# Kernel optimization log

Hardware: AMD Instinct MI355X
Metric: run time of the kernel (lower is better)

The kernel has to match this reference:

```python
import jax, jax.numpy as jnp
import numpy as np
import math

TOPK = 13
ALPHA = 1.0
BETA = 6.0
EPS = 1e-9
NUM_CLASSES = 80
BG = NUM_CLASSES
IMG = 640.0


def _make_centers():
    # YOLO-style anchor-free grid at strides 8/16/32 for a 640x640 image -> L=8400
    pts = []
    for s, g in [(8, 80), (16, 40), (32, 20)]:
        xs = (np.arange(g) + 0.5) * s
        xv, yv = np.meshgrid(xs, xs)
        pts.append(np.stack([xv.ravel(), yv.ravel()], axis=-1))
    return jnp.asarray(np.concatenate(pts, 0), jnp.float32)


def _rand_boxes(kc, kw, shape, wmin, wmax):
    c = jax.random.uniform(kc, shape + (2,), minval=0.0, maxval=IMG)
    wh = jax.random.uniform(kw, shape + (2,), minval=wmin, maxval=wmax)
    return jnp.concatenate([c - wh / 2, c + wh / 2], axis=-1)


def setup_inputs() -> dict:
    key = jax.random.key(0)
    ks = jax.random.split(key, 8)
    B, L, C, n = 32, 8400, NUM_CLASSES, 64
    centers = _make_centers()                       # (L,2)
    pred_scores = jax.random.uniform(ks[0], (B, L, C))
    # predicted boxes centered near the grid cells
    noise = jax.random.normal(ks[1], (B, L, 2)) * 8.0
    pwh = jax.random.uniform(ks[2], (B, L, 2), minval=4.0, maxval=128.0)
    pc = centers[None] + noise
    pred_bboxes = jnp.concatenate([pc - pwh / 2, pc + pwh / 2], axis=-1)
    gt_bboxes = _rand_boxes(ks[3], ks[4], (B, n), 8.0, 256.0)
    gt_labels = jax.random.randint(ks[5], (B, n, 1), 0, NUM_CLASSES).astype(jnp.int32)
    counts = jax.random.randint(ks[6], (B,), 1, n + 1)
    pad_gt_mask = (jnp.arange(n)[None, :] < counts[:, None]).astype(jnp.float32)[..., None]
    return {"pred_scores": pred_scores, "pred_bboxes": pred_bboxes,
            "cell_centers_scaled": centers, "gt_labels": gt_labels,
            "gt_bboxes": gt_bboxes, "pad_gt_mask": pad_gt_mask}


def _ciou(b1, b2, eps=1e-7):
    # pairwise complete IoU: b1 (n,4) gt, b2 (L,4) pred -> (n,L). Matches torchvision.complete_box_iou.
    a1 = (b1[:, 2] - b1[:, 0]) * (b1[:, 3] - b1[:, 1])
    a2 = (b2[:, 2] - b2[:, 0]) * (b2[:, 3] - b2[:, 1])
    lt = jnp.maximum(b1[:, None, :2], b2[None, :, :2])
    rb = jnp.minimum(b1[:, None, 2:], b2[None, :, 2:])
    wh = jnp.clip(rb - lt, 0)
    inter = wh[..., 0] * wh[..., 1]
    union = a1[:, None] + a2[None, :] - inter
    iou = inter / union
    lti = jnp.minimum(b1[:, None, :2], b2[None, :, :2])
    rbi = jnp.maximum(b1[:, None, 2:], b2[None, :, 2:])
    whi = jnp.clip(rbi - lti, 0)
    diag2 = whi[..., 0] ** 2 + whi[..., 1] ** 2 + eps
    cx1 = (b1[:, 0] + b1[:, 2]) / 2; cy1 = (b1[:, 1] + b1[:, 3]) / 2
    cx2 = (b2[:, 0] + b2[:, 2]) / 2; cy2 = (b2[:, 1] + b2[:, 3]) / 2
    dist2 = (cx1[:, None] - cx2[None, :]) ** 2 + (cy1[:, None] - cy2[None, :]) ** 2
    diou = iou - dist2 / diag2
    w1 = b1[:, 2] - b1[:, 0]; h1 = b1[:, 3] - b1[:, 1]
    w2 = b2[:, 2] - b2[:, 0]; h2 = b2[:, 3] - b2[:, 1]
    v = (4.0 / math.pi ** 2) * (jnp.arctan(w1 / h1)[:, None] - jnp.arctan(w2 / h2)[None, :]) ** 2
    alpha = jax.lax.stop_gradient(v / (1 - iou + v + eps))
    return diou - alpha * v


def reference(pred_scores, pred_bboxes, cell_centers_scaled, gt_labels, gt_bboxes, pad_gt_mask):
    B, L, C = pred_scores.shape
    n = gt_bboxes.shape[1]
    # --- points-inside-gt check: (B,n,L) ---
    x = cell_centers_scaled[None, None, :, 0]
    y = cell_centers_scaled[None, None, :, 1]
    bb = gt_bboxes[:, :, None, :]
    ltrb_min = jnp.minimum(jnp.minimum(x - bb[..., 0], y - bb[..., 1]),
                           jnp.minimum(bb[..., 2] - x, bb[..., 3] - y))
    is_in_gts = (ltrb_min > EPS).astype(gt_bboxes.dtype)        # (B,n,L)
    # --- CIoU between each gt and each pred box ---
    ious = jax.vmap(_ciou)(gt_bboxes, pred_bboxes)              # (B,n,L)
    ious = jnp.clip(jnp.nan_to_num(ious, nan=0.0), 0)
    ious = ious * pad_gt_mask * is_in_gts
    # --- gather class score of each gt's label for every cell ---
    ps_t = jnp.swapaxes(pred_scores, 1, 2)                      # (B,C,L)
    gl = gt_labels.astype(jnp.int32)                            # (B,n,1)
    bbox_cls_scores = jnp.take_along_axis(ps_t, jnp.broadcast_to(gl, (B, n, L)), axis=1)
    alignment_metrics = bbox_cls_scores ** ALPHA * ious ** BETA # (B,n,L)
    # --- topk per gt, one-hot-sum style membership ---
    _, topk_idxs = jax.lax.top_k(alignment_metrics, TOPK)       # (B,n,TOPK)
    topk_mask = jnp.broadcast_to(pad_gt_mask > 0, topk_idxs.shape)
    topk_idxs = jnp.where(topk_mask, topk_idxs, 0)
    bi = jnp.arange(B)[:, None, None]
    ni = jnp.arange(n)[None, :, None]
    cnt = jnp.zeros((B, n, L), jnp.int32).at[bi, ni, topk_idxs].add(1)
    is_in_topk = jnp.where(cnt > 1, 0, cnt).astype(alignment_metrics.dtype)
    mask_positive = is_in_topk * is_in_gts * pad_gt_mask        # (B,n,L)
    mask_positive_sum = mask_positive.sum(axis=1)               # (B,L)
    # --- resolve cells assigned to multiple gts by max IoU (unconditional == torch's data-dependent branch) ---
    is_max_iou = (ious == ious.max(axis=1, keepdims=True)).astype(ious.dtype)
    mask_positive = jnp.where(mask_positive_sum[:, None, :] > 1, is_max_iou, mask_positive)
    mask_positive_sum = mask_positive.sum(axis=1)
    assigned_gt_index = jnp.argmax(mask_positive, axis=1)       # (B,L)
    assigned_labels = jnp.take_along_axis(gl[..., 0], assigned_gt_index, axis=1)
    assigned_labels = jnp.where(mask_positive_sum > 0, assigned_labels, BG)
    assigned_bboxes = jnp.take_along_axis(gt_bboxes, assigned_gt_index[..., None], axis=1)  # (B,L,4)
    assigned_scores = jax.nn.one_hot(assigned_labels, NUM_CLASSES + 1, dtype=pred_scores.dtype)[:, :, :NUM_CLASSES]
    # --- rescale scores by normalized alignment metric ---
    am = alignment_metrics * mask_positive
    max_metrics = am.max(axis=-1, keepdims=True)
    max_ious = (ious * mask_positive).max(axis=-1, keepdims=True)
    am = am / (max_metrics + EPS) * max_ious
    norm = am.max(axis=1)[..., None]                            # (B,L,1)
    assigned_scores = assigned_scores * norm
    foreground_mask = mask_positive_sum > 0
    return assigned_labels, assigned_bboxes, assigned_scores, foreground_mask
```

## Files before the change

### kernel.cpp

```cpp
#include <hip/hip_runtime.h>

#define BATCH 32
#define LANCH 8400
#define NCLS  80
#define NGT   64
#define TOPK  13
#define NCHUNK 33
#define CAP   2048

struct GtLds {
  float4 box[NGT];
  float  ga[NGT], gcx[NGT], gcy[NGT], atg[NGT], padf[NGT];
  int    lab[NGT];
};

__device__ __forceinline__ void load_gt(GtLds& s, int b,
    const float* gt_bboxes, const int* gt_labels, const float* pad_mask, int t)
{
  if (t < NGT) {
    float4 g = reinterpret_cast<const float4*>(gt_bboxes)[b * NGT + t];
    s.box[t] = g;
    float gw = g.z - g.x, gh = g.w - g.y;
    s.ga[t]  = gw * gh;
    s.gcx[t] = (g.x + g.z) * 0.5f;
    s.gcy[t] = (g.y + g.w) * 0.5f;
    s.atg[t] = atanf(gw / gh);
    s.padf[t] = pad_mask[b * NGT + t];
    s.lab[t]  = gt_labels[b * NGT + t];
  }
}

__device__ __forceinline__ float ciou_core(
    float4 pb, float pa, float pcx, float pcy, float atp,
    float4 gb, float ga, float gcx, float gcy, float atg)
{
  float iw = fmaxf(fminf(gb.z, pb.z) - fmaxf(gb.x, pb.x), 0.f);
  float ih = fmaxf(fminf(gb.w, pb.w) - fmaxf(gb.y, pb.y), 0.f);
  float inter = iw * ih;
  float uni   = ga + pa - inter;
  float iou   = inter / uni;
  float wi = fmaxf(fmaxf(gb.z, pb.z) - fminf(gb.x, pb.x), 0.f);
  float hi = fmaxf(fmaxf(gb.w, pb.w) - fminf(gb.y, pb.y), 0.f);
  float diag2 = wi * wi + hi * hi + 1e-7f;
  float dx = gcx - pcx, dy = gcy - pcy;
  float diou = iou - (dx * dx + dy * dy) / diag2;
  float dat = atg - atp;
  float v = 0.40528473456935109f * dat * dat;
  float alpha = v / (1.f - iou + v + 1e-7f);
  return fmaxf(diou - alpha * v, 0.f);
}

__device__ __forceinline__ float masked_ciou(
    float4 pb, float pa, float pcx, float pcy, float atp, float2 cc,
    float4 gb, float ga, float gcx, float gcy, float atg, float padf)
{
  float ltrb = fminf(fminf(cc.x - gb.x, cc.y - gb.y),
                     fminf(gb.z - cc.x, gb.w - cc.y));
  if (!(ltrb > 1e-9f) || padf == 0.f) return 0.f;
  return ciou_core(pb, pa, pcx, pcy, atp, gb, ga, gcx, gcy, atg);
}

__device__ __forceinline__ unsigned long long umax64(unsigned long long a,
                                                     unsigned long long b)
{ return a > b ? a : b; }

__global__ __launch_bounds__(64) void k_rowtopk(
    const float* __restrict__ pred_scores,
    const float* __restrict__ pred_bboxes,
    const float* __restrict__ centers,
    const int*   __restrict__ gt_labels,
    const float* __restrict__ gt_bboxes,
    const float* __restrict__ pad_mask,
    unsigned long long* __restrict__ mask64)
{
  const int bg = blockIdx.x;
  if (pad_mask[bg] == 0.f) return;
  const int b = bg >> 6, g = bg & 63, lane = threadIdx.x;

  __shared__ unsigned long long s_keys[CAP];
  __shared__ int s_winl[TOPK];

  const float4 gt = reinterpret_cast<const float4*>(gt_bboxes)[bg];
  const int   lab = gt_labels[bg];
  const float gw = gt.z - gt.x, gh = gt.w - gt.y;
  const float ga = gw * gh;
  const float gcx = (gt.x + gt.z) * 0.5f, gcy = (gt.y + gt.w) * 0.5f;
  const float atg = atanf(gw / gh);

  const int gdim[3] = {80, 40, 20};
  const int base[3] = {0, 6400, 8000};
  const float inv[3] = {0.125f, 0.0625f, 0.03125f};
  int i0[3], j0[3], w_[3], cum[4]; cum[0] = 0;
  for (int k = 0; k < 3; ++k) {
    int a0 = (int)floorf(gt.x * inv[k] - 0.5f) - 1; a0 = a0 < 0 ? 0 : a0;
    int a1 = (int)ceilf (gt.z * inv[k] - 0.5f) + 1; a1 = a1 > gdim[k] - 1 ? gdim[k] - 1 : a1;
    int b0 = (int)floorf(gt.y * inv[k] - 0.5f) - 1; b0 = b0 < 0 ? 0 : b0;
    int b1 = (int)ceilf (gt.w * inv[k] - 0.5f) + 1; b1 = b1 > gdim[k] - 1 ? gdim[k] - 1 : b1;
    i0[k] = a0; j0[k] = b0;
    int ww = a1 >= a0 ? a1 - a0 + 1 : 0;
    int hh = b1 >= b0 ? b1 - b0 + 1 : 0;
    w_[k] = ww;
    cum[k + 1] = cum[k] + ww * hh;
  }
  const int total = cum[3];
  const float2* cc2 = reinterpret_cast<const float2*>(centers);
  const float4* pb4 = reinterpret_cast<const float4*>(pred_bboxes) + (size_t)b * LANCH;
  const float*  sc  = pred_scores + (size_t)b * LANCH * NCLS + lab;

  int cnt = 0;
  const unsigned long long lmask = (1ull << lane) - 1ull;
  const int iters = (total + 63) >> 6;
  for (int it = 0; it < iters; ++it) {
    const int c = it * 64 + lane;
    bool valid = false;
    unsigned long long key = 0;
    if (c < total) {
      int k = (c >= cum[1]) + (c >= cum[2]);
      int r = c - cum[k];
      int di = r % w_[k], dj = r / w_[k];
      int l = base[k] + (j0[k] + dj) * gdim[k] + (i0[k] + di);
      float2 cc = cc2[l];
      float ltrb = fminf(fminf(cc.x - gt.x, cc.y - gt.y),
                         fminf(gt.z - cc.x, gt.w - cc.y));
      if (ltrb > 1e-9f) {
        float4 pb = pb4[l];
        float pw = pb.z - pb.x, ph = pb.w - pb.y, pa = pw * ph;
        float pcx = (pb.x + pb.z) * 0.5f, pcy = (pb.y + pb.w) * 0.5f;
        float atp = atanf(pw / ph);
        float io = ciou_core(pb, pa, pcx, pcy, atp, gt, ga, gcx, gcy, atg);
        float t2 = io * io;
        float met = sc[(size_t)l * NCLS] * (t2 * t2 * t2);
        if (met > 0.f) {
          valid = true;
          key = ((unsigned long long)__float_as_uint(met) << 32)
              | (unsigned int)(0x7FFFFFFF - l);
        }
      }
    }
    unsigned long long bal = __ballot(valid);
    if (valid) s_keys[cnt + __popcll(bal & lmask)] = key;
    cnt += __popcll(bal);
  }
  const int nnz  = cnt;
  const int npos = nnz < TOPK ? nnz : TOPK;

  unsigned long long mybest = 0;
  for (int i = lane; i < nnz; i += 64) mybest = umax64(mybest, s_keys[i]);

  for (int it = 0; it < npos; ++it) {
    unsigned long long k = mybest;
    #pragma unroll
    for (int off = 32; off > 0; off >>= 1) {
      unsigned long long o = __shfl_xor(k, off);
      if (o > k) k = o;
    }
    if (lane == 0) s_winl[it] = 0x7FFFFFFF - (int)(unsigned int)(k & 0xFFFFFFFFu);
    if (mybest == k) {
      mybest = 0;
      for (int i = lane; i < nnz; i += 64) {
        unsigned long long v = s_keys[i];
        if (v == k) { s_keys[i] = 0; v = 0; }
        mybest = umax64(mybest, v);
      }
    }
  }
  if (lane == 0 && npos < TOPK) {
    int found = npos;
    for (int l = 0; found < TOPK && l < LANCH; ++l) {
      bool taken = false;
      for (int k = 0; k < npos; ++k) if (s_winl[k] == l) taken = true;
      if (!taken) s_winl[found++] = l;
    }
  }
  __syncthreads();
  if (lane < TOPK) {
    int l = s_winl[lane];
    float2 cc = cc2[l];
    float ltrb = fminf(fminf(cc.x - gt.x, cc.y - gt.y),
                       fminf(gt.z - cc.x, gt.w - cc.y));
    if (ltrb > 1e-9f)
      atomicOr(&mask64[(size_t)b * LANCH + l], 1ull << g);
  }
}

__global__ __launch_bounds__(256) void k_resolve(
    const float* __restrict__ pred_scores,
    const float* __restrict__ pred_bboxes,
    const float* __restrict__ centers,
    const int*   __restrict__ gt_labels,
    const float* __restrict__ gt_bboxes,
    const float* __restrict__ pad_mask,
    unsigned long long* __restrict__ mask64,
    float*       __restrict__ ws_mm,
    float*       __restrict__ ws_mi)
{
  __shared__ GtLds s;
  const int b = blockIdx.y, t = threadIdx.x;
  load_gt(s, b, gt_bboxes, gt_labels, pad_mask, t);
  __syncthreads();
  const int l = blockIdx.x * 256 + t;
  if (l >= LANCH) return;
  const int idx = b * LANCH + l;

  unsigned long long mb = mask64[idx];
  if (mb == 0ull) return;
  const int sum1 = __popcll(mb);

  const float4 pb = reinterpret_cast<const float4*>(pred_bboxes)[(size_t)b * LANCH + l];
  const float2 cc = reinterpret_cast<const float2*>(centers)[l];
  const float pw = pb.z - pb.x, ph = pb.w - pb.y;
  const float pa = pw * ph;
  const float pcx = (pb.x + pb.z) * 0.5f, pcy = (pb.y + pb.w) * 0.5f;
  const float atp = atanf(pw / ph);
  const float* srow = pred_scores + ((size_t)b * LANCH + l) * NCLS;

  unsigned long long fb = mb;
  if (sum1 > 1) {
    float mx = 0.f;
    unsigned long long eq = 0;
    for (int g = 0; g < NGT; ++g) {
      if (s.padf[g] == 0.f) break;
      float io = masked_ciou(pb, pa, pcx, pcy, atp, cc, s.box[g],
                             s.ga[g], s.gcx[g], s.gcy[g], s.atg[g], s.padf[g]);
      if (io > mx)       { mx = io; eq = 1ull << g; }
      else if (io == mx) { eq |= 1ull << g; }
    }
    fb = eq;
    mask64[idx] = eq;
  }

  unsigned long long bits = fb;
  while (bits) {
    int g = __ffsll((unsigned long long)bits) - 1;
    bits &= bits - 1;
    float io = masked_ciou(pb, pa, pcx, pcy, atp, cc, s.box[g],
                           s.ga[g], s.gcx[g], s.gcy[g], s.atg[g], s.padf[g]);
    float t2 = io * io;
    float met = srow[s.lab[g]] * (t2 * t2 * t2);
    atomicMax(reinterpret_cast<int*>(ws_mm + b * NGT + g), __float_as_int(met));
    atomicMax(reinterpret_cast<int*>(ws_mi + b * NGT + g), __float_as_int(io));
  }
}

__global__ __launch_bounds__(256) void k_write(
    const float* __restrict__ pred_scores,
    const float* __restrict__ pred_bboxes,
    const float* __restrict__ centers,
    const int*   __restrict__ gt_labels,
    const float* __restrict__ gt_bboxes,
    const float* __restrict__ pad_mask,
    const unsigned long long* __restrict__ mask64,
    const float* __restrict__ ws_mm,
    const float* __restrict__ ws_mi,
    float*       __restrict__ out_labels,
    float*       __restrict__ out_bboxes,
    float*       __restrict__ out_fg,
    float*       __restrict__ out_scores)
{
  __shared__ GtLds s;
  __shared__ float smm[NGT], smi[NGT];
  __shared__ float s_norm[256];
  __shared__ int   s_lab[256];
  const int b = blockIdx.y, t = threadIdx.x;
  load_gt(s, b, gt_bboxes, gt_labels, pad_mask, t);
  if (t < NGT) { smm[t] = ws_mm[b * NGT + t]; smi[t] = ws_mi[b * NGT + t]; }
  __syncthreads();
  const int l0 = blockIdx.x * 256;
  const int l  = l0 + t;
  const bool act = (l < LANCH);

  float norm = 0.f;
  int   lab  = NCLS;
  if (act) {
    const int idx = b * LANCH + l;
    unsigned long long bits = mask64[idx];
    if (bits != 0ull) {
      const float4 pb = reinterpret_cast<const float4*>(pred_bboxes)[(size_t)b * LANCH + l];
      const float2 cc = reinterpret_cast<const float2*>(centers)[l];
      const float pw = pb.z - pb.x, ph = pb.w - pb.y;
      const float pa = pw * ph;
      const float pcx = (pb.x + pb.z) * 0.5f, pcy = (pb.y + pb.w) * 0.5f;
      const float atp = atanf(pw / ph);
      const float* srow = pred_scores + ((size_t)b * LANCH + l) * NCLS;
      const int first = __ffsll((unsigned long long)bits) - 1;
      lab = s.lab[first];
      unsigned long long bb = bits;
      while (bb) {
        int g = __ffsll((unsigned long long)bb) - 1;
        bb &= bb - 1;
        float io = masked_ciou(pb, pa, pcx, pcy, atp, cc, s.box[g],
                               s.ga[g], s.gcx[g], s.gcy[g], s.atg[g], s.padf[g]);
        float t2 = io * io;
        float met = srow[s.lab[g]] * (t2 * t2 * t2);
        norm = fmaxf(norm, met / (smm[g] + 1e-9f) * smi[g]);
      }
      out_labels[idx] = (float)lab;
      reinterpret_cast<float4*>(out_bboxes)[idx] = s.box[first];
      out_fg[idx] = 1.f;
    } else {
      out_labels[idx] = (float)NCLS;
      reinterpret_cast<float4*>(out_bboxes)[idx] = s.box[0];
      out_fg[idx] = 0.f;
    }
  }
  s_norm[t] = norm;
  s_lab[t]  = lab;
  __syncthreads();

  const int QC = NCLS / 4;
  float4* tile = reinterpret_cast<float4*>(out_scores + ((size_t)b * LANCH + l0) * NCLS);
  const int amax = (LANCH - l0) < 256 ? (LANCH - l0) : 256;
  #pragma unroll
  for (int k = 0; k < QC; ++k) {
    int p = k * 256 + t;
    int a = p / QC, c4 = p - a * QC;
    if (a < amax) {
      float4 wv = make_float4(0.f, 0.f, 0.f, 0.f);
      int la = s_lab[a], base = c4 * 4;
      if (la >= base && la < base + 4) (&wv.x)[la - base] = s_norm[a];
      tile[p] = wv;
    }
  }
}

extern "C" void kernel_launch(void* const* d_in, const int* in_sizes, int n_in,
                              void* d_out, int out_size, void* d_ws, size_t ws_size,
                              hipStream_t stream) {
  const float* pred_scores = (const float*)d_in[0];
  const float* pred_bboxes = (const float*)d_in[1];
  const float* centers     = (const float*)d_in[2];
  const int*   gt_labels   = (const int*)  d_in[3];
  const float* gt_bboxes   = (const float*)d_in[4];
  const float* pad_mask    = (const float*)d_in[5];

  char* ws = (char*)d_ws;
  unsigned long long* mask64 = (unsigned long long*)ws;
  float* ws_mm = (float*)(ws + (size_t)BATCH * LANCH * 8);
  float* ws_mi = ws_mm + BATCH * NGT;
  const size_t zero_bytes = (size_t)BATCH * LANCH * 8 + 2 * BATCH * NGT * sizeof(float);

  float* out        = (float*)d_out;
  float* out_labels = out;
  float* out_bboxes = out + (size_t)BATCH * LANCH;
  float* out_scores = out + (size_t)BATCH * LANCH * 5;
  float* out_fg     = out + (size_t)BATCH * LANCH * 5 + (size_t)BATCH * LANCH * NCLS;

  hipMemsetAsync(ws, 0, zero_bytes, stream);

  k_rowtopk<<<BATCH * NGT, 64, 0, stream>>>(pred_scores, pred_bboxes, centers,
      gt_labels, gt_bboxes, pad_mask, mask64);

  dim3 grid(NCHUNK, BATCH);
  k_resolve<<<grid, 256, 0, stream>>>(pred_scores, pred_bboxes, centers,
      gt_labels, gt_bboxes, pad_mask, mask64, ws_mm, ws_mi);

  k_write<<<grid, 256, 0, stream>>>(pred_scores, pred_bboxes, centers,
      gt_labels, gt_bboxes, pad_mask, mask64, ws_mm, ws_mi,
      out_labels, out_bboxes, out_fg, out_scores);
}
```

Measured before the change: 230.3 us.

## Resolve per-batch masks in LDS and pack results for a lean write kernel

```diff
diff --git a/kernel.cpp b/kernel.cpp
--- a/kernel.cpp
+++ b/kernel.cpp
@@ -71,11 +71,11 @@
     const int*   __restrict__ gt_labels,
     const float* __restrict__ gt_bboxes,
     const float* __restrict__ pad_mask,
-    unsigned long long* __restrict__ mask64)
+    int*         __restrict__ ws_top)
 {
   const int bg = blockIdx.x;
   if (pad_mask[bg] == 0.f) return;
-  const int b = bg >> 6, g = bg & 63, lane = threadIdx.x;
+  const int b = bg >> 6, lane = threadIdx.x;
 
   __shared__ unsigned long long s_keys[CAP];
   __shared__ int s_winl[TOPK];
@@ -178,8 +178,7 @@
     float2 cc = cc2[l];
     float ltrb = fminf(fminf(cc.x - gt.x, cc.y - gt.y),
                        fminf(gt.z - cc.x, gt.w - cc.y));
-    if (ltrb > 1e-9f)
-      atomicOr(&mask64[(size_t)b * LANCH + l], 1ull << g);
+    ws_top[bg * 16 + lane] = l | ((ltrb > 1e-9f) ? 0x40000000 : 0);
   }
 }
 
@@ -190,118 +189,129 @@
     const int*   __restrict__ gt_labels,
     const float* __restrict__ gt_bboxes,
     const float* __restrict__ pad_mask,
-    unsigned long long* __restrict__ mask64,
-    float*       __restrict__ ws_mm,
-    float*       __restrict__ ws_mi)
-{
+    const int*   __restrict__ ws_top,
+    unsigned long long* __restrict__ ws_pack)
+{
+  __shared__ unsigned long long s_mask[LANCH];
   __shared__ GtLds s;
-  const int b = blockIdx.y, t = threadIdx.x;
+  __shared__ int s_mm[NGT], s_mi[NGT];
+  const int b = blockIdx.x, t = threadIdx.x;
   load_gt(s, b, gt_bboxes, gt_labels, pad_mask, t);
-  __syncthreads();
-  const int l = blockIdx.x * 256 + t;
-  if (l >= LANCH) return;
-  const int idx = b * LANCH + l;
-
-  unsigned long long mb = mask64[idx];
-  if (mb == 0ull) return;
-  const int sum1 = __popcll(mb);
-
-  const float4 pb = reinterpret_cast<const float4*>(pred_bboxes)[(size_t)b * LANCH + l];
-  const float2 cc = reinterpret_cast<const float2*>(centers)[l];
-  const float pw = pb.z - pb.x, ph = pb.w - pb.y;
-  const float pa = pw * ph;
-  const float pcx = (pb.x + pb.z) * 0.5f, pcy = (pb.y + pb.w) * 0.5f;
-  const float atp = atanf(pw / ph);
-  const float* srow = pred_scores + ((size_t)b * LANCH + l) * NCLS;
-
-  unsigned long long fb = mb;
-  if (sum1 > 1) {
-    float mx = 0.f;
-    unsigned long long eq = 0;
-    for (int g = 0; g < NGT; ++g) {
-      if (s.padf[g] == 0.f) break;
+  if (t < NGT) { s_mm[t] = 0; s_mi[t] = 0; }
+  for (int i = t; i < LANCH; i += 256) s_mask[i] = 0ull;
+  __syncthreads();
+
+  for (int p = t; p < NGT * TOPK; p += 256) {
+    int g = p / TOPK, k = p - g * TOPK;
+    if (s.padf[g] == 0.f) continue;
+    int e = ws_top[(b * NGT + g) * 16 + k];
+    if (e & 0x40000000) atomicOr(&s_mask[e & 0x3FFF], 1ull << g);
+  }
+  __syncthreads();
+
+  const float2* cc2 = reinterpret_cast<const float2*>(centers);
+  const float4* pb4 = reinterpret_cast<const float4*>(pred_bboxes) + (size_t)b * LANCH;
+
+  for (int l = t; l < LANCH; l += 256) {
+    unsigned long long mb = s_mask[l];
+    if (!mb) continue;
+    const float4 pb = pb4[l];
+    const float2 cc = cc2[l];
+    const float pw = pb.z - pb.x, ph = pb.w - pb.y;
+    const float pa = pw * ph;
+    const float pcx = (pb.x + pb.z) * 0.5f, pcy = (pb.y + pb.w) * 0.5f;
+    const float atp = atanf(pw / ph);
+    const float* srow = pred_scores + ((size_t)b * LANCH + l) * NCLS;
+
+    unsigned long long fb = mb;
+    if (__popcll(mb) > 1) {
+      float mx = 0.f;
+      unsigned long long eq = 0;
+      for (int g = 0; g < NGT; ++g) {
+        if (s.padf[g] == 0.f) break;
+        float io = masked_ciou(pb, pa, pcx, pcy, atp, cc, s.box[g],
+                               s.ga[g], s.gcx[g], s.gcy[g], s.atg[g], s.padf[g]);
+        if (io > mx)       { mx = io; eq = 1ull << g; }
+        else if (io == mx) { eq |= 1ull << g; }
+      }
+      fb = eq;
+      s_mask[l] = eq;
+    }
+    unsigned long long bits = fb;
+    while (bits) {
+      int g = __ffsll((unsigned long long)bits) - 1;
+      bits &= bits - 1;
       float io = masked_ciou(pb, pa, pcx, pcy, atp, cc, s.box[g],
                              s.ga[g], s.gcx[g], s.gcy[g], s.atg[g], s.padf[g]);
-      if (io > mx)       { mx = io; eq = 1ull << g; }
-      else if (io == mx) { eq |= 1ull << g; }
-    }
-    fb = eq;
-    mask64[idx] = eq;
-  }
-
-  unsigned long long bits = fb;
-  while (bits) {
-    int g = __ffsll((unsigned long long)bits) - 1;
-    bits &= bits - 1;
-    float io = masked_ciou(pb, pa, pcx, pcy, atp, cc, s.box[g],
-                           s.ga[g], s.gcx[g], s.gcy[g], s.atg[g], s.padf[g]);
-    float t2 = io * io;
-    float met = srow[s.lab[g]] * (t2 * t2 * t2);
-    atomicMax(reinterpret_cast<int*>(ws_mm + b * NGT + g), __float_as_int(met));
-    atomicMax(reinterpret_cast<int*>(ws_mi + b * NGT + g), __float_as_int(io));
-  }
-}
-
-__global__ __launch_bounds__(256) void k_write(
-    const float* __restrict__ pred_scores,
-    const float* __restrict__ pred_bboxes,
-    const float* __restrict__ centers,
-    const int*   __restrict__ gt_labels,
-    const float* __restrict__ gt_bboxes,
-    const float* __restrict__ pad_mask,
-    const unsigned long long* __restrict__ mask64,
-    const float* __restrict__ ws_mm,
-    const float* __restrict__ ws_mi,
-    float*       __restrict__ out_labels,
-    float*       __restrict__ out_bboxes,
-    float*       __restrict__ out_fg,
-    float*       __restrict__ out_scores)
-{
-  __shared__ GtLds s;
-  __shared__ float smm[NGT], smi[NGT];
-  __shared__ float s_norm[256];
-  __shared__ int   s_lab[256];
-  const int b = blockIdx.y, t = threadIdx.x;
-  load_gt(s, b, gt_bboxes, gt_labels, pad_mask, t);
-  if (t < NGT) { smm[t] = ws_mm[b * NGT + t]; smi[t] = ws_mi[b * NGT + t]; }
-  __syncthreads();
-  const int l0 = blockIdx.x * 256;
-  const int l  = l0 + t;
-  const bool act = (l < LANCH);
-
-  float norm = 0.f;
-  int   lab  = NCLS;
-  if (act) {
-    const int idx = b * LANCH + l;
-    unsigned long long bits = mask64[idx];
-    if (bits != 0ull) {
-      const float4 pb = reinterpret_cast<const float4*>(pred_bboxes)[(size_t)b * LANCH + l];
-      const float2 cc = reinterpret_cast<const float2*>(centers)[l];
+      float t2 = io * io;
+      float met = srow[s.lab[g]] * (t2 * t2 * t2);
+      atomicMax(&s_mm[g], __float_as_int(met));
+      atomicMax(&s_mi[g], __float_as_int(io));
+    }
+  }
+  __syncthreads();
+
+  for (int l = t; l < LANCH; l += 256) {
+    unsigned long long mb = s_mask[l];
+    unsigned long long pk = (unsigned long long)NCLS << 16;
+    if (mb) {
+      const float4 pb = pb4[l];
+      const float2 cc = cc2[l];
       const float pw = pb.z - pb.x, ph = pb.w - pb.y;
       const float pa = pw * ph;
       const float pcx = (pb.x + pb.z) * 0.5f, pcy = (pb.y + pb.w) * 0.5f;
       const float atp = atanf(pw / ph);
       const float* srow = pred_scores + ((size_t)b * LANCH + l) * NCLS;
-      const int first = __ffsll((unsigned long long)bits) - 1;
-      lab = s.lab[first];
-      unsigned long long bb = bits;
-      while (bb) {
-        int g = __ffsll((unsigned long long)bb) - 1;
-        bb &= bb - 1;
+      const int first = __ffsll((unsigned long long)mb) - 1;
+      float norm = 0.f;
+      unsigned long long bits = mb;
+      while (bits) {
+        int g = __ffsll((unsigned long long)bits) - 1;
+        bits &= bits - 1;
         float io = masked_ciou(pb, pa, pcx, pcy, atp, cc, s.box[g],
                                s.ga[g], s.gcx[g], s.gcy[g], s.atg[g], s.padf[g]);
         float t2 = io * io;
         float met = srow[s.lab[g]] * (t2 * t2 * t2);
-        norm = fmaxf(norm, met / (smm[g] + 1e-9f) * smi[g]);
+        norm = fmaxf(norm,
+                     met / (__int_as_float(s_mm[g]) + 1e-9f) * __int_as_float(s_mi[g]));
       }
-      out_labels[idx] = (float)lab;
-      reinterpret_cast<float4*>(out_bboxes)[idx] = s.box[first];
-      out_fg[idx] = 1.f;
-    } else {
-      out_labels[idx] = (float)NCLS;
-      reinterpret_cast<float4*>(out_bboxes)[idx] = s.box[0];
-      out_fg[idx] = 0.f;
-    }
+      pk = ((unsigned long long)__float_as_uint(norm) << 32)
+         | ((unsigned long long)s.lab[first] << 16)
+         | ((unsigned long long)first << 8) | 1ull;
+    }
+    ws_pack[(size_t)b * LANCH + l] = pk;
+  }
+}
+
+__global__ __launch_bounds__(256) void k_write(
+    const float* __restrict__ gt_bboxes,
+    const unsigned long long* __restrict__ ws_pack,
+    float*       __restrict__ out_labels,
+    float*       __restrict__ out_bboxes,
+    float*       __restrict__ out_fg,
+    float*       __restrict__ out_scores)
+{
+  __shared__ float4 s_box[NGT];
+  __shared__ float  s_norm[256];
+  __shared__ int    s_lab[256];
+  const int b = blockIdx.y, t = threadIdx.x;
+  if (t < NGT) s_box[t] = reinterpret_cast<const float4*>(gt_bboxes)[b * NGT + t];
+  __syncthreads();
+  const int l0 = blockIdx.x * 256;
+  const int l  = l0 + t;
+  const bool act = (l < LANCH);
+
+  float norm = 0.f;
+  int   lab  = NCLS;
+  if (act) {
+    const int idx = b * LANCH + l;
+    const unsigned long long pk = ws_pack[idx];
+    norm = __uint_as_float((unsigned int)(pk >> 32));
+    lab  = (int)((pk >> 16) & 0xFFFF);
+    const int first = (int)((pk >> 8) & 0xFF);
+    out_labels[idx] = (float)lab;
+    reinterpret_cast<float4*>(out_bboxes)[idx] = s_box[first];
+    out_fg[idx] = (float)(pk & 1ull);
   }
   s_norm[t] = norm;
   s_lab[t]  = lab;
@@ -334,10 +344,9 @@
   const float* pad_mask    = (const float*)d_in[5];
 
   char* ws = (char*)d_ws;
-  unsigned long long* mask64 = (unsigned long long*)ws;
-  float* ws_mm = (float*)(ws + (size_t)BATCH * LANCH * 8);
-  float* ws_mi = ws_mm + BATCH * NGT;
-  const size_t zero_bytes = (size_t)BATCH * LANCH * 8 + 2 * BATCH * NGT * sizeof(float);
+  int* ws_top = (int*)ws;
+  unsigned long long* ws_pack =
+      (unsigned long long*)(ws + (size_t)BATCH * NGT * 16 * 4);
 
   float* out        = (float*)d_out;
   float* out_labels = out;
@@ -345,16 +354,13 @@
   float* out_scores = out + (size_t)BATCH * LANCH * 5;
   float* out_fg     = out + (size_t)BATCH * LANCH * 5 + (size_t)BATCH * LANCH * NCLS;
 
-  hipMemsetAsync(ws, 0, zero_bytes, stream);
-
   k_rowtopk<<<BATCH * NGT, 64, 0, stream>>>(pred_scores, pred_bboxes, centers,
-      gt_labels, gt_bboxes, pad_mask, mask64);
+      gt_labels, gt_bboxes, pad_mask, ws_top);
+
+  k_resolve<<<BATCH, 256, 0, stream>>>(pred_scores, pred_bboxes, centers,
+      gt_labels, gt_bboxes, pad_mask, ws_top, ws_pack);
 
   dim3 grid(NCHUNK, BATCH);
-  k_resolve<<<grid, 256, 0, stream>>>(pred_scores, pred_bboxes, centers,
-      gt_labels, gt_bboxes, pad_mask, mask64, ws_mm, ws_mi);
-
-  k_write<<<grid, 256, 0, stream>>>(pred_scores, pred_bboxes, centers,
-      gt_labels, gt_bboxes, pad_mask, mask64, ws_mm, ws_mi,
+  k_write<<<grid, 256, 0, stream>>>(gt_bboxes, ws_pack,
       out_labels, out_bboxes, out_fg, out_scores);
 }
```

New measurement: 545.2 us. 2.37x slower.
